# Optimization experiments

Hardware: AMD Instinct MI355X
Metric: run time of the kernel (lower is better)

Reference implementation:

```python
import jax, jax.numpy as jnp
import numpy as np

B, S, D = 16, 2048, 128

def setup_inputs() -> dict:
    key = jax.random.key(0)
    k1, k2, k3 = jax.random.split(key, 3)
    return {
        "query": jax.random.normal(k1, (B, S, D), dtype=jnp.float32),
        "key": jax.random.normal(k2, (B, S, D), dtype=jnp.float32),
        "value": jax.random.normal(k3, (B, S, D), dtype=jnp.float32),
    }

def reference(query, key, value):
    dq = query.shape[-1]
    dk = key.shape[-1]
    # custom scale: sqrt(Dq) + sqrt(Dk - Dq); with Dq == Dk this is sqrt(Dq)
    inv_scale = np.sqrt(dq) + np.sqrt(dk - dq)
    qk = jnp.einsum("bqd,bkd->bqk", query, key) / jnp.float32(inv_scale)
    attn = jax.nn.softmax(qk, axis=-1)  # dropout_p=0 -> identity
    return jnp.einsum("bqk,bkd->bqd", attn, value)
```

## Files before the change

kernel.cpp:

```cpp
#include <hip/hip_runtime.h>
#include <stdint.h>

#define Bn 16
#define Sn 2048
#define Dn 128
#define QBLK 64
#define KVBLK 64
#define NTHR 256
#define NT (Sn / KVBLK)

typedef __attribute__((ext_vector_type(4))) float f32x4;
typedef __attribute__((ext_vector_type(16))) float f32x16;
typedef __attribute__((ext_vector_type(8))) short bf16x8;
typedef __attribute__((ext_vector_type(2))) unsigned int u32x2;

#define SMEM_BYTES 33792

__device__ __forceinline__ uint32_t f2bf_u(float f) {
  return (__float_as_uint(f) + 0x8000u) >> 16;
}
__device__ __forceinline__ uint32_t pk2(float a, float b) {
  return f2bf_u(a) | (f2bf_u(b) << 16);
}

__global__ __launch_bounds__(256) void cvt_k(const float* __restrict__ K,
                                             unsigned short* __restrict__ Kb) {
  const int g = blockIdx.x * 256 + threadIdx.x;
  const int c = g & 15, k = (g >> 4) & 63;
  const int t = (g >> 10) & 31, b = g >> 15;
  const float* src = K + ((size_t)b * Sn + t * 64 + k) * Dn + c * 8;
  const float4 a = *(const float4*)src;
  const float4 d = *(const float4*)(src + 4);
  uint4 o;
  o.x = pk2(a.x, a.y); o.y = pk2(a.z, a.w);
  o.z = pk2(d.x, d.y); o.w = pk2(d.z, d.w);
  const uint32_t off = (uint32_t)(k * 256 + c * 16) ^ ((uint32_t)(k & 7) << 4);
  *(uint4*)((char*)Kb + ((size_t)b * 32 + t) * 16384 + off) = o;
}

__global__ __launch_bounds__(256) void tr_v(const float* __restrict__ V,
                                            unsigned short* __restrict__ Vf) {
  __shared__ unsigned short lds[64 * 130];
  const int tid = threadIdx.x;
  const int b = blockIdx.x >> 5;
  const int t = blockIdx.x & 31;
  const float* src = V + ((size_t)b * Sn + t * 64) * Dn;
#pragma unroll
  for (int it = 0; it < 8; ++it) {
    const int gr = it * 256 + tid;
    const int k = gr >> 5, g4 = gr & 31;
    const float4 v = ((const float4*)src)[gr];
    unsigned short* p = &lds[k * 130 + g4 * 4];
    p[0] = (unsigned short)f2bf_u(v.x);
    p[1] = (unsigned short)f2bf_u(v.y);
    p[2] = (unsigned short)f2bf_u(v.z);
    p[3] = (unsigned short)f2bf_u(v.w);
  }
  __syncthreads();
  char* dst = (char*)Vf + (size_t)blockIdx.x * 16384;
#pragma unroll
  for (int it = 0; it < 4; ++it) {
    const int g = it * 256 + tid;
    const int lane = g & 63, f3 = (g >> 6) & 7, h = g >> 9;
    const int d = (f3 >> 1) * 32 + (lane & 31);
    const int k0 = 32 * h + (f3 & 1) * 16 + 8 * (lane >> 5);
    uint4 o;
    o.x = (uint32_t)lds[(k0 + 0) * 130 + d] | ((uint32_t)lds[(k0 + 1) * 130 + d] << 16);
    o.y = (uint32_t)lds[(k0 + 2) * 130 + d] | ((uint32_t)lds[(k0 + 3) * 130 + d] << 16);
    o.z = (uint32_t)lds[(k0 + 4) * 130 + d] | ((uint32_t)lds[(k0 + 5) * 130 + d] << 16);
    o.w = (uint32_t)lds[(k0 + 6) * 130 + d] | ((uint32_t)lds[(k0 + 7) * 130 + d] << 16);
    *(uint4*)(dst + g * 16) = o;
  }
}

__global__ __launch_bounds__(NTHR, 2) void attn_fwd(
    const float* __restrict__ Q, const unsigned short* __restrict__ Kb,
    const unsigned short* __restrict__ Vf, float* __restrict__ O) {
  __shared__ uint4 smem_[SMEM_BYTES / 16];
  char* smem = (char*)smem_;

  const int tid = threadIdx.x;
  const int lane = tid & 63;
  const int w = tid >> 6;
  const int qw = w & 1;
  const int h = w >> 1;
  const int hi = lane >> 5;
  const int ql = lane & 31;

  const int i = blockIdx.x;
  const int j = i >> 3;
  const int b = (i & 7) + 8 * (j & 1);
  const int q0 = (j >> 1) * QBLK;
  const int qg = q0 + qw * 32 + ql;

  const float qscale = 0.08838834764831845f * 1.44269504088896340736f;
  bf16x8 qf[8];
  {
    const float* qrow = Q + (size_t)(b * Sn + qg) * Dn;
#pragma unroll
    for (int dk = 0; dk < 8; ++dk) {
      const int d0 = dk * 16 + hi * 8;
      const float4 a = *(const float4*)(qrow + d0);
      const float4 d = *(const float4*)(qrow + d0 + 4);
      bf16x8 q8;
      q8[0] = (short)f2bf_u(a.x * qscale); q8[1] = (short)f2bf_u(a.y * qscale);
      q8[2] = (short)f2bf_u(a.z * qscale); q8[3] = (short)f2bf_u(a.w * qscale);
      q8[4] = (short)f2bf_u(d.x * qscale); q8[5] = (short)f2bf_u(d.y * qscale);
      q8[6] = (short)f2bf_u(d.z * qscale); q8[7] = (short)f2bf_u(d.w * qscale);
      qf[dk] = q8;
    }
  }

  f32x16 o[4];
#pragma unroll
  for (int dt = 0; dt < 4; ++dt) {
#pragma unroll
    for (int jj = 0; jj < 16; ++jj) o[dt][jj] = 0.f;
  }
  float m_r = -1.0e30f, l_r = 0.f;

  const char* Kg = (const char*)(Kb + (size_t)b * Sn * Dn);
  const char* Vg = (const char*)(Vf + (size_t)b * Sn * Dn);

#define STAGE_K(t_, dstoff_)                                                   \
  {                                                                            \
    const char* gsrc = Kg + (size_t)(t_)*16384 + w * 4096 + lane * 16;         \
    char* ldst = smem + (dstoff_) + w * 4096;                                  \
    _Pragma("unroll") for (int it = 0; it < 4; ++it) {                         \
      __builtin_amdgcn_global_load_lds(                                        \
          (const __attribute__((address_space(1))) uint32_t*)(gsrc + it * 1024),\
          (__attribute__((address_space(3))) uint32_t*)(ldst + it * 1024),     \
          16, 0, 0);                                                           \
    }                                                                          \
  }

  STAGE_K(0, 0)
  __syncthreads();

  for (int t = 0; t < NT; ++t) {
    const uint32_t cb = (uint32_t)(t & 1) * 16384;
    if (t < NT - 1) STAGE_K(t + 1, 16384 - cb)

    bf16x8 vfr[8];
    {
      const char* vt = Vg + (size_t)t * 16384 + h * 8192 + lane * 16;
#pragma unroll
      for (int f3 = 0; f3 < 8; ++f3)
        vfr[f3] = *(const bf16x8*)(vt + f3 * 1024);
    }

    f32x16 s;
#pragma unroll
    for (int jj = 0; jj < 16; ++jj) s[jj] = 0.f;
    __builtin_amdgcn_s_setprio(1);
#pragma unroll
    for (int dk = 0; dk < 8; ++dk) {
      const uint32_t koff =
          (uint32_t)((32 * h + ql) * 256 + dk * 32 + hi * 16) ^
          ((uint32_t)(ql & 7) << 4);
      bf16x8 a = *(const bf16x8*)(smem + cb + koff);
      s = __builtin_amdgcn_mfma_f32_32x32x16_bf16(a, qf[dk], s, 0, 0, 0);
    }
    __builtin_amdgcn_s_setprio(0);

    float x0 = fmaxf(fmaxf(s[0], s[1]), fmaxf(s[2], s[3]));
    float x1 = fmaxf(fmaxf(s[4], s[5]), fmaxf(s[6], s[7]));
    float x2 = fmaxf(fmaxf(s[8], s[9]), fmaxf(s[10], s[11]));
    float x3 = fmaxf(fmaxf(s[12], s[13]), fmaxf(s[14], s[15]));
    float pm = fmaxf(fmaxf(x0, x1), fmaxf(x2, x3));
    pm = fmaxf(pm, __shfl_xor(pm, 32, 64));

    if (!__all(pm <= m_r + 8.0f)) {
      const float mnew = fmaxf(m_r, pm);
      const float alpha = __builtin_amdgcn_exp2f(m_r - mnew);
      l_r *= alpha;
#pragma unroll
      for (int dt = 0; dt < 4; ++dt) o[dt] *= alpha;
      m_r = mnew;
    }

#pragma unroll
    for (int jj = 0; jj < 16; ++jj) s[jj] = __builtin_amdgcn_exp2f(s[jj] - m_r);
    {
      float r0 = 0.f, r1 = 0.f, r2 = 0.f, r3 = 0.f;
#pragma unroll
      for (int jj = 0; jj < 4; ++jj) {
        r0 += s[jj]; r1 += s[4 + jj]; r2 += s[8 + jj]; r3 += s[12 + jj];
      }
      float rsum = (r0 + r1) + (r2 + r3);
      l_r += rsum + __shfl_xor(rsum, 32, 64);
    }

    uint32_t own[4][2];
#pragma unroll
    for (int mm = 0; mm < 4; ++mm) {
      own[mm][0] = pk2(s[4 * mm + 0], s[4 * mm + 1]);
      own[mm][1] = pk2(s[4 * mm + 2], s[4 * mm + 3]);
    }
    uint32_t rcv[2][2];
#pragma unroll
    for (int jj = 0; jj < 2; ++jj)
#pragma unroll
      for (int e = 0; e < 2; ++e) {
        uint32_t sel = hi ? own[2 * jj][e] : own[2 * jj + 1][e];
        rcv[jj][e] = (uint32_t)__shfl_xor((int)sel, 32, 64);
      }
    bf16x8 pb[2];
#pragma unroll
    for (int ks = 0; ks < 2; ++ks) {
      union { uint32_t u[4]; bf16x8 v; } tt;
      tt.u[0] = hi ? rcv[ks][0] : own[2 * ks][0];
      tt.u[1] = hi ? rcv[ks][1] : own[2 * ks][1];
      tt.u[2] = hi ? own[2 * ks + 1][0] : rcv[ks][0];
      tt.u[3] = hi ? own[2 * ks + 1][1] : rcv[ks][1];
      pb[ks] = tt.v;
    }

    __builtin_amdgcn_s_setprio(1);
#pragma unroll
    for (int dt = 0; dt < 4; ++dt) {
#pragma unroll
      for (int ks = 0; ks < 2; ++ks) {
        o[dt] = __builtin_amdgcn_mfma_f32_32x32x16_bf16(vfr[dt * 2 + ks], pb[ks],
                                                        o[dt], 0, 0, 0);
      }
    }
    __builtin_amdgcn_s_setprio(0);

    __syncthreads();
  }

  char* xch = smem + qw * 16896;
  if (h) {
#pragma unroll
    for (int dt = 0; dt < 4; ++dt) {
#pragma unroll
      for (int q2 = 0; q2 < 4; ++q2) {
        float4 v;
        v.x = o[dt][4 * q2 + 0]; v.y = o[dt][4 * q2 + 1];
        v.z = o[dt][4 * q2 + 2]; v.w = o[dt][4 * q2 + 3];
        *(float4*)(xch + (dt * 4 + q2) * 1024 + lane * 16) = v;
      }
    }
    *(float2*)(xch + 16384 + lane * 8) = make_float2(m_r, l_r);
  }
  __syncthreads();
  if (!h) {
    const float2 ml1v = *(const float2*)(xch + 16384 + lane * 8);
    const float M = fmaxf(m_r, ml1v.x);
    const float w0 = __builtin_amdgcn_exp2f(m_r - M);
    const float w1 = __builtin_amdgcn_exp2f(ml1v.x - M);
    const float inv = 1.0f / (l_r * w0 + ml1v.y * w1);
    const float s0 = w0 * inv, s1 = w1 * inv;
    float* orow = O + (size_t)(b * Sn + qg) * Dn;
#pragma unroll
    for (int dt = 0; dt < 4; ++dt) {
#pragma unroll
      for (int q2 = 0; q2 < 4; ++q2) {
        const float4 o1v =
            *(const float4*)(xch + (dt * 4 + q2) * 1024 + lane * 16);
        float4 v;
        v.x = o[dt][4 * q2 + 0] * s0 + o1v.x * s1;
        v.y = o[dt][4 * q2 + 1] * s0 + o1v.y * s1;
        v.z = o[dt][4 * q2 + 2] * s0 + o1v.z * s1;
        v.w = o[dt][4 * q2 + 3] * s0 + o1v.w * s1;
        *(float4*)(orow + dt * 32 + q2 * 8 + hi * 4) = v;
      }
    }
  }
}

extern "C" void kernel_launch(void* const* d_in, const int* in_sizes, int n_in,
                              void* d_out, int out_size, void* d_ws, size_t ws_size,
                              hipStream_t stream) {
  (void)in_sizes; (void)n_in; (void)out_size; (void)ws_size;
  const float* Q = (const float*)d_in[0];
  const float* K = (const float*)d_in[1];
  const float* V = (const float*)d_in[2];
  float* O = (float*)d_out;

  unsigned short* Kb = (unsigned short*)d_ws;
  unsigned short* Vf = Kb + (size_t)Bn * Sn * Dn;

  cvt_k<<<dim3(2048, 1, 1), dim3(256, 1, 1), 0, stream>>>(K, Kb);
  tr_v<<<dim3(Bn * 32, 1, 1), dim3(256, 1, 1), 0, stream>>>(V, Vf);
  attn_fwd<<<dim3((Sn / QBLK) * Bn, 1, 1), dim3(NTHR, 1, 1), 0, stream>>>(
      Q, Kb, Vf, O);
}
```

Before: 69.03 us.

## Load K as pre-laid-out MFMA fragments directly from global, drop LDS staging

The K preprocessing kernel now writes bf16 K in a per-lane MFMA fragment layout, built through an LDS transpose like V. The attention kernel then loads K fragments straight from global (L2) into registers instead of staging them through double-buffered LDS with global_load_lds. This also removes the per-iteration block barrier and unrolls the KV loop by two. The aim is to cut LDS traffic and synchronisation stalls, at the cost of more register pressure and fully exposed global-load latency with no explicit prefetch.

```diff
diff --git a/kernel.cpp b/kernel.cpp
--- a/kernel.cpp
+++ b/kernel.cpp
@@ -23,28 +23,45 @@
   return f2bf_u(a) | (f2bf_u(b) << 16);
 }
 
-__global__ __launch_bounds__(256) void cvt_k(const float* __restrict__ K,
-                                             unsigned short* __restrict__ Kb) {
-  const int g = blockIdx.x * 256 + threadIdx.x;
-  const int c = g & 15, k = (g >> 4) & 63;
-  const int t = (g >> 10) & 31, b = g >> 15;
-  const float* src = K + ((size_t)b * Sn + t * 64 + k) * Dn + c * 8;
-  const float4 a = *(const float4*)src;
-  const float4 d = *(const float4*)(src + 4);
-  uint4 o;
-  o.x = pk2(a.x, a.y); o.y = pk2(a.z, a.w);
-  o.z = pk2(d.x, d.y); o.w = pk2(d.z, d.w);
-  const uint32_t off = (uint32_t)(k * 256 + c * 16) ^ ((uint32_t)(k & 7) << 4);
-  *(uint4*)((char*)Kb + ((size_t)b * 32 + t) * 16384 + off) = o;
+__global__ __launch_bounds__(256) void tr_k(const float* __restrict__ K,
+                                            unsigned short* __restrict__ Kf) {
+  __shared__ unsigned short lds[64 * 136];
+  const int tid = threadIdx.x;
+  const float* src = K + (size_t)blockIdx.x * (64 * Dn);
+#pragma unroll
+  for (int it = 0; it < 8; ++it) {
+    const int gr = it * 256 + tid;
+    const int k = gr >> 5, g4 = gr & 31;
+    const float4 v = ((const float4*)src)[gr];
+    unsigned short* p = &lds[k * 136 + g4 * 4];
+    p[0] = (unsigned short)f2bf_u(v.x);
+    p[1] = (unsigned short)f2bf_u(v.y);
+    p[2] = (unsigned short)f2bf_u(v.z);
+    p[3] = (unsigned short)f2bf_u(v.w);
+  }
+  __syncthreads();
+  char* dst = (char*)Kf + (size_t)blockIdx.x * 16384;
+#pragma unroll
+  for (int it = 0; it < 4; ++it) {
+    const int g = it * 256 + tid;
+    const int lane = g & 63, dk = (g >> 6) & 7, h = g >> 9;
+    const int row = 32 * h + (lane & 31);
+    const int d0 = dk * 16 + 8 * (lane >> 5);
+    const unsigned short* p = &lds[row * 136 + d0];
+    uint4 o;
+    o.x = (uint32_t)p[0] | ((uint32_t)p[1] << 16);
+    o.y = (uint32_t)p[2] | ((uint32_t)p[3] << 16);
+    o.z = (uint32_t)p[4] | ((uint32_t)p[5] << 16);
+    o.w = (uint32_t)p[6] | ((uint32_t)p[7] << 16);
+    *(uint4*)(dst + g * 16) = o;
+  }
 }
 
 __global__ __launch_bounds__(256) void tr_v(const float* __restrict__ V,
                                             unsigned short* __restrict__ Vf) {
   __shared__ unsigned short lds[64 * 130];
   const int tid = threadIdx.x;
-  const int b = blockIdx.x >> 5;
-  const int t = blockIdx.x & 31;
-  const float* src = V + ((size_t)b * Sn + t * 64) * Dn;
+  const float* src = V + (size_t)blockIdx.x * (64 * Dn);
 #pragma unroll
   for (int it = 0; it < 8; ++it) {
     const int gr = it * 256 + tid;
@@ -74,7 +91,7 @@
 }
 
 __global__ __launch_bounds__(NTHR, 2) void attn_fwd(
-    const float* __restrict__ Q, const unsigned short* __restrict__ Kb,
+    const float* __restrict__ Q, const unsigned short* __restrict__ Kf,
     const unsigned short* __restrict__ Vf, float* __restrict__ O) {
   __shared__ uint4 smem_[SMEM_BYTES / 16];
   char* smem = (char*)smem_;
@@ -119,34 +136,19 @@
   }
   float m_r = -1.0e30f, l_r = 0.f;
 
-  const char* Kg = (const char*)(Kb + (size_t)b * Sn * Dn);
+  const char* Kg = (const char*)(Kf + (size_t)b * Sn * Dn);
   const char* Vg = (const char*)(Vf + (size_t)b * Sn * Dn);
 
-#define STAGE_K(t_, dstoff_)                                                   \
-  {                                                                            \
-    const char* gsrc = Kg + (size_t)(t_)*16384 + w * 4096 + lane * 16;         \
-    char* ldst = smem + (dstoff_) + w * 4096;                                  \
-    _Pragma("unroll") for (int it = 0; it < 4; ++it) {                         \
-      __builtin_amdgcn_global_load_lds(                                        \
-          (const __attribute__((address_space(1))) uint32_t*)(gsrc + it * 1024),\
-          (__attribute__((address_space(3))) uint32_t*)(ldst + it * 1024),     \
-          16, 0, 0);                                                           \
-    }                                                                          \
-  }
-
-  STAGE_K(0, 0)
-  __syncthreads();
-
+#pragma unroll 2
   for (int t = 0; t < NT; ++t) {
-    const uint32_t cb = (uint32_t)(t & 1) * 16384;
-    if (t < NT - 1) STAGE_K(t + 1, 16384 - cb)
-
-    bf16x8 vfr[8];
+    bf16x8 kfr[8], vfr[8];
     {
+      const char* kt = Kg + (size_t)t * 16384 + h * 8192 + lane * 16;
       const char* vt = Vg + (size_t)t * 16384 + h * 8192 + lane * 16;
 #pragma unroll
-      for (int f3 = 0; f3 < 8; ++f3)
-        vfr[f3] = *(const bf16x8*)(vt + f3 * 1024);
+      for (int f = 0; f < 8; ++f) kfr[f] = *(const bf16x8*)(kt + f * 1024);
+#pragma unroll
+      for (int f = 0; f < 8; ++f) vfr[f] = *(const bf16x8*)(vt + f * 1024);
     }
 
     f32x16 s;
@@ -154,13 +156,8 @@
     for (int jj = 0; jj < 16; ++jj) s[jj] = 0.f;
     __builtin_amdgcn_s_setprio(1);
 #pragma unroll
-    for (int dk = 0; dk < 8; ++dk) {
-      const uint32_t koff =
-          (uint32_t)((32 * h + ql) * 256 + dk * 32 + hi * 16) ^
-          ((uint32_t)(ql & 7) << 4);
-      bf16x8 a = *(const bf16x8*)(smem + cb + koff);
-      s = __builtin_amdgcn_mfma_f32_32x32x16_bf16(a, qf[dk], s, 0, 0, 0);
-    }
+    for (int dk = 0; dk < 8; ++dk)
+      s = __builtin_amdgcn_mfma_f32_32x32x16_bf16(kfr[dk], qf[dk], s, 0, 0, 0);
     __builtin_amdgcn_s_setprio(0);
 
     float x0 = fmaxf(fmaxf(s[0], s[1]), fmaxf(s[2], s[3]));
@@ -226,10 +223,9 @@
       }
     }
     __builtin_amdgcn_s_setprio(0);
-
-    __syncthreads();
-  }
-
+  }
+
+  __syncthreads();
   char* xch = smem + qw * 16896;
   if (h) {
 #pragma unroll
@@ -279,11 +275,11 @@
   const float* V = (const float*)d_in[2];
   float* O = (float*)d_out;
 
-  unsigned short* Kb = (unsigned short*)d_ws;
-  unsigned short* Vf = Kb + (size_t)Bn * Sn * Dn;
-
-  cvt_k<<<dim3(2048, 1, 1), dim3(256, 1, 1), 0, stream>>>(K, Kb);
+  unsigned short* Kf = (unsigned short*)d_ws;
+  unsigned short* Vf = Kf + (size_t)Bn * Sn * Dn;
+
+  tr_k<<<dim3(Bn * 32, 1, 1), dim3(256, 1, 1), 0, stream>>>(K, Kf);
   tr_v<<<dim3(Bn * 32, 1, 1), dim3(256, 1, 1), 0, stream>>>(V, Vf);
   attn_fwd<<<dim3((Sn / QBLK) * Bn, 1, 1), dim3(NTHR, 1, 1), 0, stream>>>(
-      Q, Kb, Vf, O);
-}
+      Q, Kf, Vf, O);
+}
```

Result: no change. 68.20 us (-1.2%).
